# Optimization experiments

Measured on AMD Instinct MI355X. Metric: run time of the kernel, lower is better.

## Reference

```python
import jax, jax.numpy as jnp
import numpy as np

REST = 0.0
DECAY = 0.2
THRESHOLD = 0.3
BETA = 0.02
SG_WIDTH = 1.0  # rectangular surrogate-gradient window width


@jax.custom_vjp
def spike(v, thresh):
    # forward: hard threshold, y = (v > thresh)
    return (v > thresh).astype(v.dtype)


def _spike_fwd(v, thresh):
    return spike(v, thresh), (v, thresh)


def _spike_bwd(res, g):
    v, thresh = res
    # rectangular surrogate gradient w.r.t. v; threshold gets the negative
    sg = (jnp.abs(v - thresh) < (SG_WIDTH * 0.5)).astype(g.dtype) / SG_WIDTH
    gv = g * sg
    return (gv, -gv)


spike.defvjp(_spike_fwd, _spike_bwd)


def setup_inputs() -> dict:
    key = jax.random.key(0)
    k1, k2 = jax.random.split(key)
    T, B, N = 512, 64, 1024
    tx = jax.random.normal(k1, (T, B, N), dtype=jnp.float32)
    TE = jax.random.normal(k2, (N, T), dtype=jnp.float32) * 0.1  # learned temporal encoding
    return {"tx": tx, "TE": TE}


def reference(tx, TE):
    # tx: [T, B, N] time-major input; TE: [N, T] per-neuron temporal encoding
    T, B, N = tx.shape
    v0 = jnp.full((B, N), REST, tx.dtype)
    y0 = jnp.zeros((B, N), tx.dtype)
    th0 = jnp.full((B, N), THRESHOLD, tx.dtype)

    def step(carry, inp):
        v, y, th = carry
        x, te_t = inp  # x: [B, N], te_t: [N]
        th = th + v * te_t - (th - THRESHOLD) * BETA
        v = v * DECAY * (1.0 - y) + x
        y = spike(v, th)
        return (v, y, th), y

    _, ty = jax.lax.scan(step, (v0, y0, th0), (tx, TE.T))
    return ty  # [T, B, N] spike trains
```

## Files before the change

### kernel.cpp

```cpp
#include <hip/hip_runtime.h>


#define T_STEPS 512
#define BATCH   64
#define NNEUR   1024
#define BN      (BATCH * NNEUR)
#define UCHUNK  16

__global__ __launch_bounds__(256) void telif_kernel(
    const float* __restrict__ tx, const float* __restrict__ TE,
    float* __restrict__ out)
{
#pragma clang fp contract(off)

    const int flat = blockIdx.x * 256 + threadIdx.x;
    const int n = flat & (NNEUR - 1);

    const float* txp = tx + flat;
    const float* tep = TE + n * T_STEPS;
    float*       outp = out + flat;

    float v  = 0.0f;
    float y  = 0.0f;
    float th = 0.3f;

    float xc[UCHUNK], tc[UCHUNK];
    float xn[UCHUNK], tn[UCHUNK];

#pragma unroll
    for (int u = 0; u < UCHUNK; ++u)
        xc[u] = __builtin_nontemporal_load(txp + (size_t)u * BN);
#pragma unroll
    for (int u = 0; u < UCHUNK; u += 4) {
        float4 f = *reinterpret_cast<const float4*>(tep + u);
        tc[u] = f.x; tc[u + 1] = f.y; tc[u + 2] = f.z; tc[u + 3] = f.w;
    }

#pragma unroll 1
    for (int t = 0; t < T_STEPS; t += UCHUNK) {
        const int tb = t + UCHUNK;
        if (tb < T_STEPS) {
#pragma unroll
            for (int u = 0; u < UCHUNK; ++u)
                xn[u] = __builtin_nontemporal_load(txp + (size_t)(tb + u) * BN);
#pragma unroll
            for (int u = 0; u < UCHUNK; u += 4) {
                float4 f = *reinterpret_cast<const float4*>(tep + tb + u);
                tn[u] = f.x; tn[u + 1] = f.y; tn[u + 2] = f.z; tn[u + 3] = f.w;
            }
        }

#pragma unroll
        for (int u = 0; u < UCHUNK; ++u) {
            float a    = v * tc[u];
            float bsum = th + a;
            float c    = th - 0.3f;
            float d    = c * 0.02f;
            th = bsum - d;
            float e  = v * 0.2f;
            float f1 = 1.0f - y;
            float g  = e * f1;
            v = g + xc[u];
            y = (v > th) ? 1.0f : 0.0f;
            __builtin_nontemporal_store(y, outp + (size_t)(t + u) * BN);
        }

#pragma unroll
        for (int u = 0; u < UCHUNK; ++u) { xc[u] = xn[u]; tc[u] = tn[u]; }
    }
}

extern "C" void kernel_launch(void* const* d_in, const int* in_sizes, int n_in,
                              void* d_out, int out_size, void* d_ws, size_t ws_size,
                              hipStream_t stream) {
    const float* tx = (const float*)d_in[0];
    const float* TE = (const float*)d_in[1];
    float* out = (float*)d_out;
    telif_kernel<<<BN / 256, 256, 0, stream>>>(tx, TE, out);
}
```

Before: 233.4 us.

## Add producer wave streaming tx into LDS ring buffer via global_load_lds

Adds a dedicated producer wavefront per block that issues asynchronous global-to-LDS loads of tx, three chunks ahead, into a four-slot shared-memory ring. The 256 consumer threads now read x from LDS instead of holding a register double buffer, and the two roles synchronise with block barriers each chunk. The aim is deeper prefetch to hide global load latency in this latency-bound sequential scan, while freeing consumer registers. In exchange it adds 64KB of LDS per block, a barrier per chunk, and hand-tuned vmcnt waits that must match the number of outstanding loads exactly.

```diff
diff --git a/kernel.cpp b/kernel.cpp
--- a/kernel.cpp
+++ b/kernel.cpp
@@ -6,17 +6,62 @@
 #define NNEUR   1024
 #define BN      (BATCH * NNEUR)
 #define UCHUNK  16
+#define NCHUNK  (T_STEPS / UCHUNK)
+#define NSLOT   4
+#define CONS_THREADS 256
+#define BLOCK_THREADS 320
 
-__global__ __launch_bounds__(256) void telif_kernel(
+__global__ __launch_bounds__(BLOCK_THREADS) void telif_kernel(
     const float* __restrict__ tx, const float* __restrict__ TE,
     float* __restrict__ out)
 {
 #pragma clang fp contract(off)
 
-    const int flat = blockIdx.x * 256 + threadIdx.x;
+    __shared__ float buf[NSLOT][UCHUNK][CONS_THREADS];
+
+    const int tid = threadIdx.x;
+    const int blockBase = blockIdx.x * CONS_THREADS;
+
+    if (tid >= CONS_THREADS) {
+        const int lane = tid - CONS_THREADS;
+        const float* gbase = tx + blockBase + lane * 4;
+
+        auto issue_chunk = [&](int k) {
+            const int slot = k & (NSLOT - 1);
+#pragma unroll
+            for (int u = 0; u < UCHUNK; ++u) {
+                const float* g = gbase + (size_t)(k * UCHUNK + u) * BN;
+                __builtin_amdgcn_global_load_lds(
+                    (const __attribute__((address_space(1))) void*)g,
+                    (__attribute__((address_space(3))) void*)&buf[slot][u][0],
+                    16, 0, 0);
+            }
+        };
+
+        issue_chunk(0);
+        issue_chunk(1);
+        issue_chunk(2);
+        asm volatile("s_waitcnt vmcnt(32)" ::: "memory");
+        __builtin_amdgcn_sched_barrier(0);
+        __builtin_amdgcn_s_barrier();
+
+        for (int r = 0; r < NCHUNK; ++r) {
+            if (r + 3 < NCHUNK) issue_chunk(r + 3);
+            if (r <= NCHUNK - 4) {
+                asm volatile("s_waitcnt vmcnt(32)" ::: "memory");
+            } else if (r == NCHUNK - 3) {
+                asm volatile("s_waitcnt vmcnt(16)" ::: "memory");
+            } else {
+                asm volatile("s_waitcnt vmcnt(0)" ::: "memory");
+            }
+            __builtin_amdgcn_sched_barrier(0);
+            __builtin_amdgcn_s_barrier();
+        }
+        return;
+    }
+
+    const int flat = blockBase + tid;
     const int n = flat & (NNEUR - 1);
-
-    const float* txp = tx + flat;
     const float* tep = TE + n * T_STEPS;
     float*       outp = out + flat;
 
@@ -24,34 +69,30 @@
     float y  = 0.0f;
     float th = 0.3f;
 
-    float xc[UCHUNK], tc[UCHUNK];
-    float xn[UCHUNK], tn[UCHUNK];
-
-#pragma unroll
-    for (int u = 0; u < UCHUNK; ++u)
-        xc[u] = __builtin_nontemporal_load(txp + (size_t)u * BN);
+    float tc[UCHUNK], tn[UCHUNK];
 #pragma unroll
     for (int u = 0; u < UCHUNK; u += 4) {
         float4 f = *reinterpret_cast<const float4*>(tep + u);
         tc[u] = f.x; tc[u + 1] = f.y; tc[u + 2] = f.z; tc[u + 3] = f.w;
     }
+    __builtin_amdgcn_s_barrier();
 
 #pragma unroll 1
-    for (int t = 0; t < T_STEPS; t += UCHUNK) {
-        const int tb = t + UCHUNK;
-        if (tb < T_STEPS) {
-#pragma unroll
-            for (int u = 0; u < UCHUNK; ++u)
-                xn[u] = __builtin_nontemporal_load(txp + (size_t)(tb + u) * BN);
+    for (int r = 0; r < NCHUNK; ++r) {
+        const int t = r * UCHUNK;
+
+        if (r + 1 < NCHUNK) {
 #pragma unroll
             for (int u = 0; u < UCHUNK; u += 4) {
-                float4 f = *reinterpret_cast<const float4*>(tep + tb + u);
+                float4 f = *reinterpret_cast<const float4*>(tep + t + UCHUNK + u);
                 tn[u] = f.x; tn[u + 1] = f.y; tn[u + 2] = f.z; tn[u + 3] = f.w;
             }
         }
 
+        const float* xs = &buf[r & (NSLOT - 1)][0][tid];
 #pragma unroll
         for (int u = 0; u < UCHUNK; ++u) {
+            float x = xs[(size_t)u * CONS_THREADS];
             float a    = v * tc[u];
             float bsum = th + a;
             float c    = th - 0.3f;
@@ -60,13 +101,15 @@
             float e  = v * 0.2f;
             float f1 = 1.0f - y;
             float g  = e * f1;
-            v = g + xc[u];
+            v = g + x;
             y = (v > th) ? 1.0f : 0.0f;
             __builtin_nontemporal_store(y, outp + (size_t)(t + u) * BN);
         }
 
 #pragma unroll
-        for (int u = 0; u < UCHUNK; ++u) { xc[u] = xn[u]; tc[u] = tn[u]; }
+        for (int u = 0; u < UCHUNK; ++u) tc[u] = tn[u];
+
+        __builtin_amdgcn_s_barrier();
     }
 }
 
@@ -76,5 +119,5 @@
     const float* tx = (const float*)d_in[0];
     const float* TE = (const float*)d_in[1];
     float* out = (float*)d_out;
-    telif_kernel<<<BN / 256, 256, 0, stream>>>(tx, TE, out);
+    telif_kernel<<<BN / CONS_THREADS, BLOCK_THREADS, 0, stream>>>(tx, TE, out);
 }
```

Result: no change. 233.6 us (+0.1%).

## Deepen register prefetch to two chunks ahead with 4-slot ring buffer

Applied to the files above, without the earlier changes.

Replaces the double-buffered register prefetch with a 4-slot register ring buffer, issuing loads two 16-step chunks ahead and unrolling the outer loop by four so slot indices stay static. This puts more loads in flight per thread to hide HBM latency in the sequential recurrence, and drops the per-chunk register copy. It also switches tx loads from nontemporal to regular loads. The cost is more registers (about 128 floats of buffers), which could lower occupancy.

```diff
diff --git a/kernel.cpp b/kernel.cpp
--- a/kernel.cpp
+++ b/kernel.cpp
@@ -6,6 +6,7 @@
 #define NNEUR   1024
 #define BN      (BATCH * NNEUR)
 #define UCHUNK  16
+#define NCHUNK  (T_STEPS / UCHUNK)
 
 __global__ __launch_bounds__(256) void telif_kernel(
     const float* __restrict__ tx, const float* __restrict__ TE,
@@ -16,7 +17,6 @@
     const int flat = blockIdx.x * 256 + threadIdx.x;
     const int n = flat & (NNEUR - 1);
 
-    const float* txp = tx + flat;
     const float* tep = TE + n * T_STEPS;
     float*       outp = out + flat;
 
@@ -24,49 +24,57 @@
     float y  = 0.0f;
     float th = 0.3f;
 
-    float xc[UCHUNK], tc[UCHUNK];
-    float xn[UCHUNK], tn[UCHUNK];
+    float xb[4][UCHUNK], tb[4][UCHUNK];
 
 #pragma unroll
-    for (int u = 0; u < UCHUNK; ++u)
-        xc[u] = __builtin_nontemporal_load(txp + (size_t)u * BN);
+    for (int c = 0; c < 2; ++c) {
 #pragma unroll
-    for (int u = 0; u < UCHUNK; u += 4) {
-        float4 f = *reinterpret_cast<const float4*>(tep + u);
-        tc[u] = f.x; tc[u + 1] = f.y; tc[u + 2] = f.z; tc[u + 3] = f.w;
+        for (int u = 0; u < UCHUNK; ++u)
+            xb[c][u] = tx[(size_t)(c * UCHUNK + u) * BN + flat];
+#pragma unroll
+        for (int u = 0; u < UCHUNK; u += 4) {
+            float4 f = *reinterpret_cast<const float4*>(tep + c * UCHUNK + u);
+            tb[c][u] = f.x; tb[c][u+1] = f.y; tb[c][u+2] = f.z; tb[c][u+3] = f.w;
+        }
     }
 
 #pragma unroll 1
-    for (int t = 0; t < T_STEPS; t += UCHUNK) {
-        const int tb = t + UCHUNK;
-        if (tb < T_STEPS) {
+    for (int s = 0; s < NCHUNK / 4; ++s) {
 #pragma unroll
-            for (int u = 0; u < UCHUNK; ++u)
-                xn[u] = __builtin_nontemporal_load(txp + (size_t)(tb + u) * BN);
+        for (int c = 0; c < 4; ++c) {
+            const int k = s * 4 + c;
+            const int t = k * UCHUNK;
+
+            if (k + 2 < NCHUNK) {
+                const int t2 = t + 2 * UCHUNK;
 #pragma unroll
-            for (int u = 0; u < UCHUNK; u += 4) {
-                float4 f = *reinterpret_cast<const float4*>(tep + tb + u);
-                tn[u] = f.x; tn[u + 1] = f.y; tn[u + 2] = f.z; tn[u + 3] = f.w;
+                for (int u = 0; u < UCHUNK; ++u)
+                    xb[(c + 2) & 3][u] = tx[(size_t)(t2 + u) * BN + flat];
+#pragma unroll
+                for (int u = 0; u < UCHUNK; u += 4) {
+                    float4 f = *reinterpret_cast<const float4*>(tep + t2 + u);
+                    tb[(c + 2) & 3][u]     = f.x;
+                    tb[(c + 2) & 3][u + 1] = f.y;
+                    tb[(c + 2) & 3][u + 2] = f.z;
+                    tb[(c + 2) & 3][u + 3] = f.w;
+                }
+            }
+
+#pragma unroll
+            for (int u = 0; u < UCHUNK; ++u) {
+                float a    = v * tb[c][u];
+                float bsum = th + a;
+                float cc   = th - 0.3f;
+                float d    = cc * 0.02f;
+                th = bsum - d;
+                float e  = v * 0.2f;
+                float f1 = 1.0f - y;
+                float g  = e * f1;
+                v = g + xb[c][u];
+                y = (v > th) ? 1.0f : 0.0f;
+                __builtin_nontemporal_store(y, outp + (size_t)(t + u) * BN);
             }
         }
-
-#pragma unroll
-        for (int u = 0; u < UCHUNK; ++u) {
-            float a    = v * tc[u];
-            float bsum = th + a;
-            float c    = th - 0.3f;
-            float d    = c * 0.02f;
-            th = bsum - d;
-            float e  = v * 0.2f;
-            float f1 = 1.0f - y;
-            float g  = e * f1;
-            v = g + xc[u];
-            y = (v > th) ? 1.0f : 0.0f;
-            __builtin_nontemporal_store(y, outp + (size_t)(t + u) * BN);
-        }
-
-#pragma unroll
-        for (int u = 0; u < UCHUNK; ++u) { xc[u] = xn[u]; tc[u] = tn[u]; }
     }
 }
 
```

New measurement: 237.6 us. About the same (+1.8%).
